# Kernel optimization log

Hardware: AMD Instinct MI355X
Metric: run time of the kernel (lower is better)

The kernel has to match this reference:

```python
import jax, jax.numpy as jnp
import numpy as np
from jax import lax

EPS = 1e-12

def _l2norm(v, axis):
    n = jnp.linalg.norm(v, axis=axis, keepdims=True)
    return v / jnp.maximum(n, EPS)

def setup_inputs() -> dict:
    key = jax.random.key(0)
    k1, k2, k3 = jax.random.split(key, 3)
    C, H, W, K = 512, 192, 192, 64
    x = jax.random.normal(k1, (C, H, W), dtype=jnp.float32)
    conv_w = jax.random.normal(k2, (K, C), dtype=jnp.float32) * 0.05  # 1x1 conv, no bias (vladv2=False)
    centroids = jax.random.uniform(k3, (K, C), dtype=jnp.float32)
    return {"x": x, "conv_w": conv_w, "centroids": centroids}

def reference(x, conv_w, centroids):
    K = conv_w.shape[0]
    x4 = x[None]                      # [1,C,H,W]
    N, C, H, W = x4.shape
    L = H * W
    # descriptor-wise L2 normalization over channels
    x4 = _l2norm(x4, axis=1)
    # 1x1 conv -> soft assignment over clusters
    logits = jnp.einsum('kc,nchw->nkhw', conv_w, x4)
    soft = jax.nn.softmax(logits, axis=1)          # [N,K,H,W]
    sa_flat = soft.reshape(N, K, L)
    # top-2 cluster indices per location (argmax + second largest)
    _, top2 = lax.top_k(sa_flat.transpose(0, 2, 1), 2)  # [N,L,2]
    first, second = top2[..., 0], top2[..., 1]
    # unfold 3x3, padding 1: windows [N, L, K, 9] in (kh,kw) order
    pad = jnp.pad(soft, ((0, 0), (0, 0), (1, 1), (1, 1)))
    patches = jnp.stack([pad[:, :, di:di + H, dj:dj + W]
                         for di in range(3) for dj in range(3)], axis=2)  # [N,K,9,H,W]
    windows = patches.reshape(N, K, 9, L).transpose(0, 3, 1, 2)           # [N,L,K,9]
    # keep only windows of the top-2 clusters at each location
    karange = jnp.arange(K)[None, None, :]
    keep = (karange == first[:, :, None]) | (karange == second[:, :, None])  # [N,L,K]
    wsel = windows * keep[..., None].astype(windows.dtype)
    # fold (transpose of unfold): overlap-add back to [N,K,H,W]
    ws = wsel.transpose(0, 2, 3, 1).reshape(N, K, 9, H, W)
    out_pad = jnp.zeros((N, K, H + 2, W + 2), dtype=ws.dtype)
    t = 0
    for di in range(3):
        for dj in range(3):
            out_pad = out_pad.at[:, :, di:di + H, dj:dj + W].add(ws[:, :, t])
            t += 1
    weight = out_pad[:, :, 1:H + 1, 1:W + 1]
    # border mask: (min distance to border)^4
    ii = jnp.arange(H); jj = jnp.arange(W)
    mi = jnp.minimum(H - 1 - ii, ii)[:, None]
    mj = jnp.minimum(W - 1 - jj, jj)[None, :]
    m = jnp.minimum(mi, mj).astype(weight.dtype)
    m2 = m * m
    mask = m2 * m2
    weight = weight * mask[None, None]
    sa2 = weight.reshape(N, K, L)
    # per-cluster residual accumulation, vectorized (replaces the 64-iter loop)
    xf = x4.reshape(N, C, L)
    vlad = jnp.einsum('nkl,ncl->nkc', sa2, xf) - sa2.sum(-1)[..., None] * centroids[None]
    vlad = _l2norm(vlad, axis=2)               # intra-normalization
    v = vlad.reshape(N, -1)
    v = _l2norm(v, axis=1)
    return v
```

## Files before the change

kernel.cpp:

```cpp
#include <hip/hip_runtime.h>

#define HH 192
#define WW 192
#define LL (HH * WW)
#define CC 512
#define KK 64
#define EPSF 1e-12f
typedef unsigned long long ull;
typedef unsigned int uint;
typedef unsigned short ushort;

#define NCHUNK 192
#define CHUNKL (LL / NCHUNK)

typedef short bf16x8 __attribute__((ext_vector_type(8)));
typedef float f32x4 __attribute__((ext_vector_type(4)));

__device__ inline void split3(float v, ushort& h, ushort& md, ushort& lo) {
    uint b  = __float_as_uint(v);
    uint hb = b & 0xFFFF0000u;
    float r1 = v - __uint_as_float(hb);
    uint mb = __float_as_uint(r1) & 0xFFFF0000u;
    float r2 = r1 - __uint_as_float(mb);
    uint lb = __float_as_uint(r2) & 0xFFFF0000u;
    h = (ushort)(hb >> 16); md = (ushort)(mb >> 16); lo = (ushort)(lb >> 16);
}

__global__ __launch_bounds__(256) void k0_prep(const float* __restrict__ w,
                                               ushort* __restrict__ Whi,
                                               ushort* __restrict__ Wmid,
                                               ushort* __restrict__ Wlo,
                                               float* __restrict__ Szero) {
    int idx = blockIdx.x * 256 + threadIdx.x;
    int k = idx >> 9;
    int c = idx & 511;
    int s = c >> 5, w32 = c & 31, quad = w32 >> 3, j = w32 & 7;
    int kg = k >> 4, m = k & 15;
    int dst = (((s * 4 + kg) * 4 + quad) * 16 + m) * 8 + j;
    float v = w[idx];
    ushort h, md, lo;
    split3(v, h, md, lo);
    Whi[dst] = h; Wmid[dst] = md; Wlo[dst] = lo;
    if (blockIdx.x == 0 && threadIdx.x < 128) Szero[threadIdx.x] = 0.f;
}

__global__ __launch_bounds__(256) void k1_logits(const float* __restrict__ x,
                                                 const ushort* __restrict__ Whi,
                                                 const ushort* __restrict__ Wmid,
                                                 const ushort* __restrict__ Wlo,
                                                 float* __restrict__ soft,
                                                 float* __restrict__ invn,
                                                 ull* __restrict__ keep) {
    __shared__ float accL[3][32][64];
    __shared__ float ssL[3][2][64];
    int t = threadIdx.x, lane = t & 63, wid = t >> 6;
    int m = lane & 15, quad = lane >> 4;
    int pb = blockIdx.x * 32;
    int s16base = wid * 4;

    f32x4 acc[4][2];
#pragma unroll
    for (int kg = 0; kg < 4; ++kg)
#pragma unroll
        for (int cg = 0; cg < 2; ++cg) acc[kg][cg] = (f32x4){0.f, 0.f, 0.f, 0.f};
    float ssA[2] = {0.f, 0.f};

    const float* xq = x + (size_t)(wid * 128 + quad * 8) * LL + pb + m;

    bf16x8 Ah[2][4], Am[2][4], Al[2][4];
    float xv[2][2][8];

#pragma unroll
    for (int kg = 0; kg < 4; ++kg) {
        size_t off = (size_t)(((s16base * 4 + kg) * 64 + lane) * 8);
        Ah[0][kg] = *(const bf16x8*)(Whi  + off);
        Am[0][kg] = *(const bf16x8*)(Wmid + off);
        Al[0][kg] = *(const bf16x8*)(Wlo  + off);
    }
#pragma unroll
    for (int j = 0; j < 8; ++j) {
        const float* xr = xq + (size_t)j * LL;
        xv[0][0][j] = xr[0];
        xv[0][1][j] = xr[16];
    }

#pragma unroll
    for (int s = 0; s < 4; ++s) {
        const int cur = s & 1, nxt = cur ^ 1;
        if (s < 3) {
            int s16 = s16base + s + 1;
#pragma unroll
            for (int kg = 0; kg < 4; ++kg) {
                size_t off = (size_t)(((s16 * 4 + kg) * 64 + lane) * 8);
                Ah[nxt][kg] = *(const bf16x8*)(Whi  + off);
                Am[nxt][kg] = *(const bf16x8*)(Wmid + off);
                Al[nxt][kg] = *(const bf16x8*)(Wlo  + off);
            }
            const float* xp = xq + (size_t)(s + 1) * 32 * LL;
#pragma unroll
            for (int j = 0; j < 8; ++j) {
                const float* xr = xp + (size_t)j * LL;
                xv[nxt][0][j] = xr[0];
                xv[nxt][1][j] = xr[16];
            }
        }
        __builtin_amdgcn_sched_barrier(0);

        bf16x8 Bh[2], Bm[2], Bl[2];
#pragma unroll
        for (int cg = 0; cg < 2; ++cg)
#pragma unroll
            for (int j = 0; j < 8; ++j) {
                float v = xv[cur][cg][j];
                ssA[cg] = fmaf(v, v, ssA[cg]);
                ushort h, md, lo;
                split3(v, h, md, lo);
                Bh[cg][j] = (short)h; Bm[cg][j] = (short)md; Bl[cg][j] = (short)lo;
            }
#pragma unroll
        for (int kg = 0; kg < 4; ++kg)
#pragma unroll
            for (int cg = 0; cg < 2; ++cg) {
                f32x4 a = acc[kg][cg];
                a = __builtin_amdgcn_mfma_f32_16x16x32_bf16(Ah[cur][kg], Bh[cg], a, 0, 0, 0);
                a = __builtin_amdgcn_mfma_f32_16x16x32_bf16(Ah[cur][kg], Bm[cg], a, 0, 0, 0);
                a = __builtin_amdgcn_mfma_f32_16x16x32_bf16(Am[cur][kg], Bh[cg], a, 0, 0, 0);
                a = __builtin_amdgcn_mfma_f32_16x16x32_bf16(Ah[cur][kg], Bl[cg], a, 0, 0, 0);
                a = __builtin_amdgcn_mfma_f32_16x16x32_bf16(Al[cur][kg], Bh[cg], a, 0, 0, 0);
                a = __builtin_amdgcn_mfma_f32_16x16x32_bf16(Am[cur][kg], Bm[cg], a, 0, 0, 0);
                acc[kg][cg] = a;
            }
    }

    if (wid != 0) {
#pragma unroll
        for (int kg = 0; kg < 4; ++kg)
#pragma unroll
            for (int cg = 0; cg < 2; ++cg)
#pragma unroll
                for (int r = 0; r < 4; ++r)
                    accL[wid - 1][kg * 8 + cg * 4 + r][lane] = acc[kg][cg][r];
        ssL[wid - 1][0][lane] = ssA[0];
        ssL[wid - 1][1][lane] = ssA[1];
    }
    __syncthreads();
    if (wid != 0) return;
#pragma unroll
    for (int q = 0; q < 3; ++q) {
#pragma unroll
        for (int kg = 0; kg < 4; ++kg)
#pragma unroll
            for (int cg = 0; cg < 2; ++cg)
#pragma unroll
                for (int r = 0; r < 4; ++r)
                    acc[kg][cg][r] += accL[q][kg * 8 + cg * 4 + r][lane];
        ssA[0] += ssL[q][0][lane];
        ssA[1] += ssL[q][1][lane];
    }

#pragma unroll
    for (int cg = 0; cg < 2; ++cg) {
        float ssv = ssA[cg];
        ssv += __shfl_xor(ssv, 16);
        ssv += __shfl_xor(ssv, 32);
        float iv = 1.0f / fmaxf(sqrtf(ssv), EPSF);
        int px = pb + cg * 16 + m;
        if (quad == 0) invn[px] = iv;

        float lg[16];
        float M1 = -3.0e38f, M2 = -3.0e38f; int I1 = 0, I2 = 0;
#pragma unroll
        for (int kg = 0; kg < 4; ++kg)
#pragma unroll
            for (int r = 0; r < 4; ++r) {
                float v = acc[kg][cg][r] * iv;
                lg[kg * 4 + r] = v;
                int kk = kg * 16 + quad * 4 + r;
                if (v > M1)      { M2 = M1; I2 = I1; M1 = v; I1 = kk; }
                else if (v > M2) { M2 = v; I2 = kk; }
            }
#pragma unroll
        for (int st = 0; st < 2; ++st) {
            int d = 16 << st;
            float a1 = __shfl_xor(M1, d); int b1 = __shfl_xor(I1, d);
            float a2 = __shfl_xor(M2, d); int b2 = __shfl_xor(I2, d);
            if (a1 > M1 || (a1 == M1 && b1 < I1)) { M2 = M1; I2 = I1; M1 = a1; I1 = b1; }
            else if (a1 > M2 || (a1 == M2 && b1 < I2)) { M2 = a1; I2 = b1; }
            if (a2 > M1 || (a2 == M1 && b2 < I1)) { M2 = M1; I2 = I1; M1 = a2; I1 = b2; }
            else if (a2 > M2 || (a2 == M2 && b2 < I2)) { M2 = a2; I2 = b2; }
        }

        float es = 0.f;
#pragma unroll
        for (int q = 0; q < 16; ++q) { float e = __expf(lg[q] - M1); lg[q] = e; es += e; }
        es += __shfl_xor(es, 16);
        es += __shfl_xor(es, 32);
        float rs = 1.0f / es;

        float4* sp = (float4*)(soft + (size_t)px * KK + quad * 4);
#pragma unroll
        for (int kg = 0; kg < 4; ++kg) {
            float4 o;
            o.x = lg[kg * 4 + 0] * rs; o.y = lg[kg * 4 + 1] * rs;
            o.z = lg[kg * 4 + 2] * rs; o.w = lg[kg * 4 + 3] * rs;
            sp[kg * 4] = o;
        }
        if (quad == 0) keep[px] = (1ull << I1) | (1ull << I2);
    }
}

__global__ __launch_bounds__(256) void k2_weight(float* __restrict__ soft,
                                                 const ull* __restrict__ keep,
                                                 const float* __restrict__ invn,
                                                 float* __restrict__ S) {
    __shared__ float sred[4][64];
    int t = threadIdx.x, lane = t & 63, wid = t >> 6;
    int l0 = blockIdx.x * 32 + wid * 8;
    float sk = 0.f;
#pragma unroll
    for (int p = 0; p < 8; ++p) {
        int l = l0 + p;
        int i = l / WW, j = l % WW;
        int m = min(min(i, HH - 1 - i), min(j, WW - 1 - j));
        float bm = (float)m; bm *= bm; bm *= bm;
        int cnt = 0;
#pragma unroll
        for (int di = -1; di <= 1; ++di) {
            int ii = i + di;
            if (ii < 0 || ii >= HH) continue;
#pragma unroll
            for (int dj = -1; dj <= 1; ++dj) {
                int jj = j + dj;
                if (jj < 0 || jj >= WW) continue;
                ull nb = keep[ii * WW + jj];
                cnt += (int)((nb >> lane) & 1ull);
            }
        }
        float v = soft[(size_t)l * KK + lane];
        float u = v * (float)cnt * bm;
        sk += u;
        soft[(size_t)l * KK + lane] = u * invn[l];
    }
    sred[wid][lane] = sk;
    __syncthreads();
    if (wid == 0)
        atomicAdd(&S[lane], sred[0][lane] + sred[1][lane] + sred[2][lane] + sred[3][lane]);
}

__device__ inline void cvt_pair(float v0, float v1, uint& hp, uint& lp) {
    uint b0 = __float_as_uint(v0), b1 = __float_as_uint(v1);
    uint h0 = b0 & 0xFFFF0000u, h1 = b1 & 0xFFFF0000u;
    float r0 = v0 - __uint_as_float(h0);
    float r1 = v1 - __uint_as_float(h1);
    hp = (h0 >> 16) | h1;
    lp = (__float_as_uint(r0) >> 16) | (__float_as_uint(r1) & 0xFFFF0000u);
}

__global__ __launch_bounds__(256) void k3_mfma(const float* __restrict__ w2,
                                               const float* __restrict__ x,
                                               float* __restrict__ partials) {
    __shared__ ushort wa_hi[64][40], wa_lo[64][40];
    __shared__ ushort xb_hi[128][40], xb_lo[128][40];
    int chunk = blockIdx.x;
    int c0 = blockIdx.y * 128;
    int l0 = chunk * CHUNKL;
    int t = threadIdx.x, lane = t & 63, wid = t >> 6;
    int m = lane & 15, quad = lane >> 4;

    f32x4 acc[4][2];
#pragma unroll
    for (int kg = 0; kg < 4; ++kg)
#pragma unroll
        for (int cg = 0; cg < 2; ++cg) acc[kg][cg] = (f32x4){0.f, 0.f, 0.f, 0.f};

    for (int lb = 0; lb < CHUNKL; lb += 32) {
        {
            int k = t & 63, rg = t >> 6;
#pragma unroll
            for (int i = 0; i < 4; ++i) {
                int lp = rg + 4 * i;
                int gl = l0 + lb + 2 * lp;
                float v0 = w2[(size_t)gl * KK + k];
                float v1 = w2[(size_t)(gl + 1) * KK + k];
                uint hp, lq;
                cvt_pair(v0, v1, hp, lq);
                *(uint*)&wa_hi[k][2 * lp] = hp;
                *(uint*)&wa_lo[k][2 * lp] = lq;
            }
        }
        {
            int lp = t & 15, cb = t >> 4;
            int gl = l0 + lb + 2 * lp;
#pragma unroll
            for (int i = 0; i < 8; ++i) {
                int c = cb + 16 * i;
                float v0 = x[(size_t)(c0 + c) * LL + gl];
                float v1 = x[(size_t)(c0 + c) * LL + gl + 1];
                uint hp, lq;
                cvt_pair(v0, v1, hp, lq);
                *(uint*)&xb_hi[c][2 * lp] = hp;
                *(uint*)&xb_lo[c][2 * lp] = lq;
            }
        }
        __syncthreads();
        bf16x8 Ah[4], Al[4];
#pragma unroll
        for (int kg = 0; kg < 4; ++kg) {
            Ah[kg] = *(bf16x8*)&wa_hi[kg * 16 + m][quad * 8];
            Al[kg] = *(bf16x8*)&wa_lo[kg * 16 + m][quad * 8];
        }
#pragma unroll
        for (int cg = 0; cg < 2; ++cg) {
            int crow = wid * 32 + cg * 16 + m;
            bf16x8 Bh = *(bf16x8*)&xb_hi[crow][quad * 8];
            bf16x8 Bl = *(bf16x8*)&xb_lo[crow][quad * 8];
#pragma unroll
            for (int kg = 0; kg < 4; ++kg) {
                acc[kg][cg] = __builtin_amdgcn_mfma_f32_16x16x32_bf16(Ah[kg], Bh, acc[kg][cg], 0, 0, 0);
                acc[kg][cg] = __builtin_amdgcn_mfma_f32_16x16x32_bf16(Ah[kg], Bl, acc[kg][cg], 0, 0, 0);
                acc[kg][cg] = __builtin_amdgcn_mfma_f32_16x16x32_bf16(Al[kg], Bh, acc[kg][cg], 0, 0, 0);
            }
        }
        __syncthreads();
    }
    float* pp = partials + (size_t)chunk * KK * CC;
#pragma unroll
    for (int kg = 0; kg < 4; ++kg)
#pragma unroll
        for (int cg = 0; cg < 2; ++cg) {
            int cout = c0 + wid * 32 + cg * 16 + m;
#pragma unroll
            for (int r = 0; r < 4; ++r) {
                int kout = kg * 16 + quad * 4 + r;
                pp[(size_t)kout * CC + cout] = acc[kg][cg][r];
            }
        }
}

__global__ __launch_bounds__(512) void k4a_reduce(const float* __restrict__ partials,
                                                  const float* __restrict__ S,
                                                  const float* __restrict__ cent,
                                                  float* __restrict__ vlad,
                                                  float* __restrict__ rowsq) {
    __shared__ float red[512];
    int k = blockIdx.x;
    int ci = threadIdx.x & 127;
    int c = blockIdx.y * 128 + ci;
    int q = threadIdx.x >> 7;
    const float* pk = partials + (size_t)q * (NCHUNK / 4) * KK * CC + (size_t)k * CC + c;
    float s0 = 0.f, s1 = 0.f, s2 = 0.f, s3 = 0.f;
    for (int ch = 0; ch < NCHUNK / 4; ch += 4) {
        s0 += pk[(size_t)(ch + 0) * KK * CC];
        s1 += pk[(size_t)(ch + 1) * KK * CC];
        s2 += pk[(size_t)(ch + 2) * KK * CC];
        s3 += pk[(size_t)(ch + 3) * KK * CC];
    }
    red[threadIdx.x] = (s0 + s1) + (s2 + s3);
    __syncthreads();
    float vsq = 0.f;
    if (q == 0) {
        float v = red[ci] + red[ci + 128] + red[ci + 256] + red[ci + 384];
        v -= S[k] * cent[k * CC + c];
        vlad[k * CC + c] = v;
        vsq = v * v;
    }
    __syncthreads();
    red[threadIdx.x] = vsq;
    __syncthreads();
    for (int off = 256; off > 0; off >>= 1) {
        if (threadIdx.x < off) red[threadIdx.x] += red[threadIdx.x + off];
        __syncthreads();
    }
    if (threadIdx.x == 0) atomicAdd(&rowsq[k], red[0]);
}

__global__ __launch_bounds__(256) void k4c_finish(const float* __restrict__ vlad,
                                                  const float* __restrict__ rowsq,
                                                  float* __restrict__ out) {
    __shared__ float rns[64];
    int t = threadIdx.x;
    if (t < 64) {
        float tot = rowsq[t];
        float r = 1.0f / fmaxf(sqrtf(tot), EPSF);
        float contrib = tot * r * r;
#pragma unroll
        for (int off = 32; off; off >>= 1) contrib += __shfl_xor(contrib, off, 64);
        float ginv = 1.0f / fmaxf(sqrtf(contrib), EPSF);
        rns[t] = r * ginv;
    }
    __syncthreads();
    int idx4 = blockIdx.x * 256 + t;
    int k = idx4 >> 7;
    float s = rns[k];
    float4 v = ((const float4*)vlad)[idx4];
    v.x *= s; v.y *= s; v.z *= s; v.w *= s;
    ((float4*)out)[idx4] = v;
}

extern "C" void kernel_launch(void* const* d_in, const int* in_sizes, int n_in,
                              void* d_out, int out_size, void* d_ws, size_t ws_size,
                              hipStream_t stream) {
    const float* x      = (const float*)d_in[0];
    const float* conv_w = (const float*)d_in[1];
    const float* cent   = (const float*)d_in[2];
    float* out = (float*)d_out;

    float* ws    = (float*)d_ws;
    ushort* Whi  = (ushort*)ws;
    ushort* Wmid = Whi + 32768;
    ushort* Wlo  = Wmid + 32768;
    float* soft  = ws + 49152;
    float* invn  = soft + (size_t)KK * LL;
    float* S     = invn + LL;
    float* rowsq = S + KK;
    float* vlad  = rowsq + KK;
    ull*   keep  = (ull*)(vlad + 32768);
    float* partials = (float*)(keep + LL);

    k0_prep<<<(KK * CC) / 256, 256, 0, stream>>>(conv_w, Whi, Wmid, Wlo, S);
    k1_logits<<<LL / 32, 256, 0, stream>>>(x, Whi, Wmid, Wlo, soft, invn, keep);
    k2_weight<<<LL / 32, 256, 0, stream>>>(soft, keep, invn, S);
    k3_mfma<<<dim3(NCHUNK, 4), 256, 0, stream>>>(soft, x, partials);
    k4a_reduce<<<dim3(KK, 4), 512, 0, stream>>>(partials, S, cent, vlad, rowsq);
    k4c_finish<<<(KK * CC / 4) / 256, 256, 0, stream>>>(vlad, rowsq, out);
}
```

Baseline: 198.7 us.

## Emit pre-split bf16 weights in MFMA fragment layout and drop LDS staging

k2_weight now writes the weighted soft assignments as hi/lo bf16 pairs directly in the per-lane MFMA A-fragment order, instead of writing fp32 back into the soft buffer. k3_mfma then loads A fragments straight from global memory. Each wave also reads its own x B-fragments with float4 loads and splits them in registers, so the LDS tiles and both __syncthreads are gone. The aim is to remove shared-memory traffic, barriers and repeated conversion work. The cost is an extra workspace buffer and x loads that are less coalesced (8 floats per lane across 16 rows).

Result: no change. 198.3 us (-0.2%).

```diff
diff --git a/kernel.cpp b/kernel.cpp
--- a/kernel.cpp
+++ b/kernel.cpp
@@ -24,6 +24,13 @@
     float r2 = r1 - __uint_as_float(mb);
     uint lb = __float_as_uint(r2) & 0xFFFF0000u;
     h = (ushort)(hb >> 16); md = (ushort)(mb >> 16); lo = (ushort)(lb >> 16);
+}
+
+__device__ inline void split2(float v, ushort& h, ushort& lo) {
+    uint b  = __float_as_uint(v);
+    uint hb = b & 0xFFFF0000u;
+    float r = v - __uint_as_float(hb);
+    h = (ushort)(hb >> 16); lo = (ushort)(__float_as_uint(r) >> 16);
 }
 
 __global__ __launch_bounds__(256) void k0_prep(const float* __restrict__ w,
@@ -209,14 +216,17 @@
     }
 }
 
-__global__ __launch_bounds__(256) void k2_weight(float* __restrict__ soft,
+__global__ __launch_bounds__(256) void k2_weight(const float* __restrict__ soft,
                                                  const ull* __restrict__ keep,
                                                  const float* __restrict__ invn,
-                                                 float* __restrict__ S) {
+                                                 float* __restrict__ S,
+                                                 ushort* __restrict__ w2t_hi,
+                                                 ushort* __restrict__ w2t_lo) {
     __shared__ float sred[4][64];
     int t = threadIdx.x, lane = t & 63, wid = t >> 6;
     int l0 = blockIdx.x * 32 + wid * 8;
     float sk = 0.f;
+    bf16x8 hv, lv;
 #pragma unroll
     for (int p = 0; p < 8; ++p) {
         int l = l0 + p;
@@ -239,28 +249,24 @@
         float v = soft[(size_t)l * KK + lane];
         float u = v * (float)cnt * bm;
         sk += u;
-        soft[(size_t)l * KK + lane] = u * invn[l];
-    }
+        float w2v = u * invn[l];
+        ushort h, lo;
+        split2(w2v, h, lo);
+        hv[p] = (short)h; lv[p] = (short)lo;
+    }
+    size_t off = (size_t)((((l0 >> 5) * 4 + (lane >> 4)) * 64 + ((l0 >> 3) & 3) * 16 + (lane & 15)) * 8);
+    *(bf16x8*)(w2t_hi + off) = hv;
+    *(bf16x8*)(w2t_lo + off) = lv;
     sred[wid][lane] = sk;
     __syncthreads();
     if (wid == 0)
         atomicAdd(&S[lane], sred[0][lane] + sred[1][lane] + sred[2][lane] + sred[3][lane]);
 }
 
-__device__ inline void cvt_pair(float v0, float v1, uint& hp, uint& lp) {
-    uint b0 = __float_as_uint(v0), b1 = __float_as_uint(v1);
-    uint h0 = b0 & 0xFFFF0000u, h1 = b1 & 0xFFFF0000u;
-    float r0 = v0 - __uint_as_float(h0);
-    float r1 = v1 - __uint_as_float(h1);
-    hp = (h0 >> 16) | h1;
-    lp = (__float_as_uint(r0) >> 16) | (__float_as_uint(r1) & 0xFFFF0000u);
-}
-
-__global__ __launch_bounds__(256) void k3_mfma(const float* __restrict__ w2,
+__global__ __launch_bounds__(256) void k3_mfma(const ushort* __restrict__ w2t_hi,
+                                               const ushort* __restrict__ w2t_lo,
                                                const float* __restrict__ x,
                                                float* __restrict__ partials) {
-    __shared__ ushort wa_hi[64][40], wa_lo[64][40];
-    __shared__ ushort xb_hi[128][40], xb_lo[128][40];
     int chunk = blockIdx.x;
     int c0 = blockIdx.y * 128;
     int l0 = chunk * CHUNKL;
@@ -273,55 +279,40 @@
 #pragma unroll
         for (int cg = 0; cg < 2; ++cg) acc[kg][cg] = (f32x4){0.f, 0.f, 0.f, 0.f};
 
+    const float* xb = x + (size_t)(c0 + wid * 32 + m) * LL + l0 + quad * 8;
+
+#pragma unroll
     for (int lb = 0; lb < CHUNKL; lb += 32) {
-        {
-            int k = t & 63, rg = t >> 6;
-#pragma unroll
-            for (int i = 0; i < 4; ++i) {
-                int lp = rg + 4 * i;
-                int gl = l0 + lb + 2 * lp;
-                float v0 = w2[(size_t)gl * KK + k];
-                float v1 = w2[(size_t)(gl + 1) * KK + k];
-                uint hp, lq;
-                cvt_pair(v0, v1, hp, lq);
-                *(uint*)&wa_hi[k][2 * lp] = hp;
-                *(uint*)&wa_lo[k][2 * lp] = lq;
-            }
-        }
-        {
-            int lp = t & 15, cb = t >> 4;
-            int gl = l0 + lb + 2 * lp;
-#pragma unroll
-            for (int i = 0; i < 8; ++i) {
-                int c = cb + 16 * i;
-                float v0 = x[(size_t)(c0 + c) * LL + gl];
-                float v1 = x[(size_t)(c0 + c) * LL + gl + 1];
-                uint hp, lq;
-                cvt_pair(v0, v1, hp, lq);
-                *(uint*)&xb_hi[c][2 * lp] = hp;
-                *(uint*)&xb_lo[c][2 * lp] = lq;
-            }
-        }
-        __syncthreads();
+        int lstep = (l0 + lb) >> 5;
         bf16x8 Ah[4], Al[4];
 #pragma unroll
         for (int kg = 0; kg < 4; ++kg) {
-            Ah[kg] = *(bf16x8*)&wa_hi[kg * 16 + m][quad * 8];
-            Al[kg] = *(bf16x8*)&wa_lo[kg * 16 + m][quad * 8];
-        }
+            size_t off = (size_t)(((lstep * 4 + kg) * 64 + lane) * 8);
+            Ah[kg] = *(const bf16x8*)(w2t_hi + off);
+            Al[kg] = *(const bf16x8*)(w2t_lo + off);
+        }
+        bf16x8 Bh[2], Bl[2];
 #pragma unroll
         for (int cg = 0; cg < 2; ++cg) {
-            int crow = wid * 32 + cg * 16 + m;
-            bf16x8 Bh = *(bf16x8*)&xb_hi[crow][quad * 8];
-            bf16x8 Bl = *(bf16x8*)&xb_lo[crow][quad * 8];
+            const float* xr = xb + (size_t)(cg * 16) * LL + lb;
+            float4 v0 = *(const float4*)xr;
+            float4 v1 = *(const float4*)(xr + 4);
+            float vv[8] = {v0.x, v0.y, v0.z, v0.w, v1.x, v1.y, v1.z, v1.w};
+#pragma unroll
+            for (int j = 0; j < 8; ++j) {
+                ushort h, lo;
+                split2(vv[j], h, lo);
+                Bh[cg][j] = (short)h; Bl[cg][j] = (short)lo;
+            }
+        }
+#pragma unroll
+        for (int cg = 0; cg < 2; ++cg)
 #pragma unroll
             for (int kg = 0; kg < 4; ++kg) {
-                acc[kg][cg] = __builtin_amdgcn_mfma_f32_16x16x32_bf16(Ah[kg], Bh, acc[kg][cg], 0, 0, 0);
-                acc[kg][cg] = __builtin_amdgcn_mfma_f32_16x16x32_bf16(Ah[kg], Bl, acc[kg][cg], 0, 0, 0);
-                acc[kg][cg] = __builtin_amdgcn_mfma_f32_16x16x32_bf16(Al[kg], Bh, acc[kg][cg], 0, 0, 0);
-            }
-        }
-        __syncthreads();
+                acc[kg][cg] = __builtin_amdgcn_mfma_f32_16x16x32_bf16(Ah[kg], Bh[cg], acc[kg][cg], 0, 0, 0);
+                acc[kg][cg] = __builtin_amdgcn_mfma_f32_16x16x32_bf16(Ah[kg], Bl[cg], acc[kg][cg], 0, 0, 0);
+                acc[kg][cg] = __builtin_amdgcn_mfma_f32_16x16x32_bf16(Al[kg], Bh[cg], acc[kg][cg], 0, 0, 0);
+            }
     }
     float* pp = partials + (size_t)chunk * KK * CC;
 #pragma unroll
@@ -415,12 +406,14 @@
     float* rowsq = S + KK;
     float* vlad  = rowsq + KK;
     ull*   keep  = (ull*)(vlad + 32768);
-    float* partials = (float*)(keep + LL);
+    ushort* w2t_hi = (ushort*)(keep + LL);
+    ushort* w2t_lo = w2t_hi + (size_t)LL * KK;
+    float* partials = (float*)(w2t_lo + (size_t)LL * KK);
 
     k0_prep<<<(KK * CC) / 256, 256, 0, stream>>>(conv_w, Whi, Wmid, Wlo, S);
     k1_logits<<<LL / 32, 256, 0, stream>>>(x, Whi, Wmid, Wlo, soft, invn, keep);
-    k2_weight<<<LL / 32, 256, 0, stream>>>(soft, keep, invn, S);
-    k3_mfma<<<dim3(NCHUNK, 4), 256, 0, stream>>>(soft, x, partials);
+    k2_weight<<<LL / 32, 256, 0, stream>>>(soft, keep, invn, S, w2t_hi, w2t_lo);
+    k3_mfma<<<dim3(NCHUNK, 4), 256, 0, stream>>>(w2t_hi, w2t_lo, x, partials);
     k4a_reduce<<<dim3(KK, 4), 512, 0, stream>>>(partials, S, cent, vlad, rowsq);
     k4c_finish<<<(KK * CC / 4) / 256, 256, 0, stream>>>(vlad, rowsq, out);
 }
```
